# Kernel optimization log

Measured on AMD Instinct MI355X. Metric: run time of the kernel, lower is better.

## Reference

```python
import jax, jax.numpy as jnp
from jax import lax
import numpy as np

AE_THRESHOLD = 0.5


def setup_inputs() -> dict:
    key = jax.random.key(0)
    ks = jax.random.split(key, 8)
    B, C, H, W = 8, 80, 128, 128
    return {
        "tl_heat": jax.random.normal(ks[0], (B, C, H, W), jnp.float32),
        "br_heat": jax.random.normal(ks[1], (B, C, H, W), jnp.float32),
        "ct_heat": jax.random.normal(ks[2], (B, C, H, W), jnp.float32),
        "tl_tag": jax.random.normal(ks[3], (B, 1, H, W), jnp.float32),
        "br_tag": jax.random.normal(ks[4], (B, 1, H, W), jnp.float32),
        "tl_regr": jax.random.normal(ks[5], (B, 2, H, W), jnp.float32),
        "br_regr": jax.random.normal(ks[6], (B, 2, H, W), jnp.float32),
        "ct_regr": jax.random.normal(ks[7], (B, 2, H, W), jnp.float32),
        "K": 100,
        "kernel": 3,
        "num_dets": 1000,
    }


def _nms(heat, kernel):
    # maxpool NMS: keep only local maxima (SAME padding, stride 1, NCHW)
    hmax = lax.reduce_window(heat, -jnp.inf, lax.max,
                             (1, 1, kernel, kernel), (1, 1, 1, 1), 'SAME')
    return heat * (hmax == heat).astype(heat.dtype)


def _topk(scores, K):
    B, C, H, W = scores.shape
    s, inds = lax.top_k(scores.reshape(B, -1), K)  # over cat*H*W
    clses = inds // (H * W)
    inds = inds % (H * W)
    ys = (inds // W).astype(jnp.float32)
    xs = (inds % W).astype(jnp.float32)
    return s, inds, clses, ys, xs


def _gather(feat, inds):
    # NCHW -> (B, H*W, C), gather spatial rows by inds (B, K) -> (B, K, C)
    B, C, H, W = feat.shape
    f = feat.transpose(0, 2, 3, 1).reshape(B, H * W, C)
    return jnp.take_along_axis(f, inds[:, :, None], axis=1)


def reference(tl_heat, br_heat, ct_heat, tl_tag, br_tag,
              tl_regr, br_regr, ct_regr, K, kernel, num_dets):
    B, C, H, W = tl_heat.shape

    tl_heat = _nms(jax.nn.sigmoid(tl_heat), kernel)
    br_heat = _nms(jax.nn.sigmoid(br_heat), kernel)
    ct_heat = _nms(jax.nn.sigmoid(ct_heat), kernel)

    tl_s, tl_inds, tl_clses, tl_ys, tl_xs = _topk(tl_heat, K)
    br_s, br_inds, br_clses, br_ys, br_xs = _topk(br_heat, K)
    ct_s, ct_inds, ct_clses, ct_ys, ct_xs = _topk(ct_heat, K)

    tl_off = _gather(tl_regr, tl_inds)  # (B, K, 2)
    br_off = _gather(br_regr, br_inds)
    ct_off = _gather(ct_regr, ct_inds)

    # corner coords with sub-pixel offsets; broadcast to (B, K, K) pairs
    tl_xs_p = (tl_xs + tl_off[..., 0])[:, :, None]  # (B, K, 1)
    tl_ys_p = (tl_ys + tl_off[..., 1])[:, :, None]
    br_xs_p = (br_xs + br_off[..., 0])[:, None, :]  # (B, 1, K)
    br_ys_p = (br_ys + br_off[..., 1])[:, None, :]
    ct_xs_p = ct_xs + ct_off[..., 0]                # (B, K)
    ct_ys_p = ct_ys + ct_off[..., 1]

    pair = (B, K, K)
    bboxes = jnp.stack([jnp.broadcast_to(tl_xs_p, pair),
                        jnp.broadcast_to(tl_ys_p, pair),
                        jnp.broadcast_to(br_xs_p, pair),
                        jnp.broadcast_to(br_ys_p, pair)], axis=-1)  # (B,K,K,4)

    tl_emb = _gather(tl_tag, tl_inds)[:, :, 0]  # (B, K)
    br_emb = _gather(br_tag, br_inds)[:, :, 0]
    dists = jnp.abs(tl_emb[:, :, None] - br_emb[:, None, :])  # (B,K,K)

    scores = (tl_s[:, :, None] + br_s[:, None, :]) * 0.5
    reject = ((tl_clses[:, :, None] != br_clses[:, None, :])
              | (dists > AE_THRESHOLD)
              | (br_xs_p < tl_xs_p)
              | (br_ys_p < tl_ys_p))
    scores = jnp.where(reject, -jnp.ones_like(scores), scores)

    scores, inds = lax.top_k(scores.reshape(B, -1), num_dets)  # (B, num_dets)

    bboxes = jnp.take_along_axis(bboxes.reshape(B, K * K, 4),
                                 inds[:, :, None], axis=1)
    clses_full = jnp.broadcast_to(tl_clses[:, :, None], pair).reshape(B, K * K)
    clses = jnp.take_along_axis(clses_full, inds, axis=1).astype(jnp.float32)
    tl_s_full = jnp.broadcast_to(tl_s[:, :, None], pair).reshape(B, K * K)
    br_s_full = jnp.broadcast_to(br_s[:, None, :], pair).reshape(B, K * K)
    tl_sc = jnp.take_along_axis(tl_s_full, inds, axis=1)
    br_sc = jnp.take_along_axis(br_s_full, inds, axis=1)

    detections = jnp.concatenate([bboxes, scores[..., None], tl_sc[..., None],
                                  br_sc[..., None], clses[..., None]], axis=-1)
    center = jnp.stack([ct_xs_p, ct_ys_p,
                        ct_clses.astype(jnp.float32), ct_s], axis=-1)  # (B,K,4)
    return detections, center
```

## Files before the change

kernel.cpp:

```cpp
#include <hip/hip_runtime.h>
#include <cstdint>

#define NB    8
#define NC    80
#define HH    128
#define WW    128
#define HW    16384
#define CHW   1310720
#define KTOP  100
#define NDET  1000
#define NPAIR 10000
#define CAP   4096
#define ACAP  2048
#define NBINS 4096
#define VTHR  3.5f

#define OFF_CCNT   0
#define OFF_CCNT2  3072
#define OFF_HIST   6144
#define ZERO_BYTES 399360
#define OFF_THR    399360
#define OFF_CAND   399488
#define OFF_CS     1185920
#define OFF_CX     1195520
#define OFF_CY     1205120
#define OFF_CE     1214720
#define OFF_CCLS   1224320
#define WS_NEEDED  1233920

__device__ __forceinline__ float sigmoidf(float x) {
    float e = expf(-fabsf(x));
    return (x >= 0.f ? 1.f : e) / (1.f + e);
}

__global__ void __launch_bounds__(256) k_nms(
        const float* __restrict__ tl, const float* __restrict__ br,
        const float* __restrict__ ct,
        uint64_t* __restrict__ cand, int* __restrict__ ccnt) {
    __shared__ float lds[34 * WW];

    int tid = threadIdx.x;
    int bid = blockIdx.x;
    int bc = bid / 320;
    int rem_b = bid - bc * 320;
    int chan = rem_b >> 2;
    int q = rem_b & 3;
    int t = bc >> 3; int b = bc & 7;
    const float* heat = (t == 0) ? tl : (t == 1) ? br : ct;
    const float* cb = heat + (size_t)b * CHW + (size_t)chan * HW;
    int ybase = q * 32;
    const float NEG = -__builtin_inff();

    #define GADDR(K, GY) ({ int r_ = (K) >> 5; (GY) = ybase - 1 + r_; \
                            int gyc_ = min(max((GY), 0), HH - 1); \
                            cb + gyc_ * WW + (((K) & 31) << 2); })
    int gy0, gy1, gy2, gy3, gy4 = 0;
    const float* a0 = GADDR(tid,        gy0);
    const float* a1 = GADDR(tid + 256,  gy1);
    const float* a2 = GADDR(tid + 512,  gy2);
    const float* a3 = GADDR(tid + 768,  gy3);
    float4 v0 = *(const float4*)a0;
    float4 v1 = *(const float4*)a1;
    float4 v2 = *(const float4*)a2;
    float4 v3 = *(const float4*)a3;
    float4 v4 = make_float4(0.f, 0.f, 0.f, 0.f);
    if (tid < 64) { const float* a4 = GADDR(tid + 1024, gy4); v4 = *(const float4*)a4; }
    #undef GADDR
    #define PIN(v) asm volatile("" : "+v"(v.x), "+v"(v.y), "+v"(v.z), "+v"(v.w))
    PIN(v0); PIN(v1); PIN(v2); PIN(v3); PIN(v4);
    #undef PIN

    #define STORE(K, V, GY) { \
        float4 vv = (V); \
        if ((GY) < 0 || (GY) > HH - 1) vv = make_float4(NEG, NEG, NEG, NEG); \
        *(float4*)&lds[(((K) >> 5) * WW) + (((K) & 31) << 2)] = vv; }
    STORE(tid,        v0, gy0)
    STORE(tid + 256,  v1, gy1)
    STORE(tid + 512,  v2, gy2)
    STORE(tid + 768,  v3, gy3)
    if (tid < 64) STORE(tid + 1024, v4, gy4)
    #undef STORE
    __syncthreads();

    int rg = tid >> 5;
    int tile_x = (tid & 31) << 2;
    int lrow = 1 + rg * 4;
    float4 A = *(const float4*)&lds[(lrow - 1) * WW + tile_x];
    float4 B = *(const float4*)&lds[lrow * WW + tile_x];
    int ccbase = bc * 32;
    uint64_t* cd = cand + (size_t)bc * CAP;
    int ibase = chan * HW + (ybase + rg * 4) * WW + tile_x;

    #pragma unroll
    for (int j = 0; j < 4; ++j) {
        float4 C = *(const float4*)&lds[(lrow + j + 1) * WW + tile_x];
        float c0 = fmaxf(fmaxf(A.x, B.x), C.x);
        float c1 = fmaxf(fmaxf(A.y, B.y), C.y);
        float c2 = fmaxf(fmaxf(A.z, B.z), C.z);
        float c3 = fmaxf(fmaxf(A.w, B.w), C.w);
        float cl = __shfl_up(c3, 1);
        float cr = __shfl_down(c0, 1);
        if (tile_x == 0)      cl = NEG;
        if (tile_x == WW - 4) cr = NEG;
        float w0 = fmaxf(fmaxf(cl, c0), c1);
        float w1 = fmaxf(fmaxf(c0, c1), c2);
        float w2 = fmaxf(fmaxf(c1, c2), c3);
        float w3 = fmaxf(fmaxf(c2, c3), cr);

        #define EMIT(Wm, V, P) \
            if ((Wm) == (V) && (V) >= VTHR) { \
                uint32_t bt = __float_as_uint(sigmoidf(V)); \
                int pos = atomicAdd(&ccnt[ccbase], 1); \
                if (pos < CAP) \
                    cd[pos] = ((uint64_t)bt << 32) | \
                              (uint32_t)(~(uint32_t)(ibase + j * WW + (P))); \
            }
        EMIT(w0, B.x, 0)
        EMIT(w1, B.y, 1)
        EMIT(w2, B.z, 2)
        EMIT(w3, B.w, 3)
        #undef EMIT
        A = B; B = C;
    }
}

__device__ uint64_t key_at(const float* __restrict__ hb, int i) {
    float v = hb[i];
    int rem = i & (HW - 1);
    int y = rem >> 7, x = rem & (WW - 1);
    bool mx = true;
    if (y > 0) {
        if (x > 0      && hb[i - WW - 1] > v) mx = false;
        if (              hb[i - WW    ] > v) mx = false;
        if (x < WW - 1 && hb[i - WW + 1] > v) mx = false;
    }
    if (x > 0      && hb[i - 1] > v) mx = false;
    if (x < WW - 1 && hb[i + 1] > v) mx = false;
    if (y < HH - 1) {
        if (x > 0      && hb[i + WW - 1] > v) mx = false;
        if (              hb[i + WW    ] > v) mx = false;
        if (x < WW - 1 && hb[i + WW + 1] > v) mx = false;
    }
    if (!mx) return 0;
    return ((uint64_t)__float_as_uint(sigmoidf(v)) << 32) | (uint32_t)(~(uint32_t)i);
}

__device__ __forceinline__ bool fast_ok(const int* ccnt, int bc) {
    int n = ccnt[bc * 32];
    return (n >= KTOP) && (n <= CAP);
}

__global__ void __launch_bounds__(256) fb_hist(
        const int* __restrict__ ccnt,
        const float* __restrict__ tl, const float* __restrict__ br,
        const float* __restrict__ ct, uint32_t* __restrict__ hist) {
    int bc = blockIdx.y;
    if (fast_ok(ccnt, bc)) return;
    __shared__ uint32_t lh[NBINS];
    for (int i = threadIdx.x; i < NBINS; i += 256) lh[i] = 0;
    __syncthreads();
    int t = bc >> 3; int b = bc & 7;
    const float* heat = (t == 0) ? tl : (t == 1) ? br : ct;
    const float* hb = heat + (size_t)b * CHW;
    for (int i = blockIdx.x * 256 + threadIdx.x; i < CHW; i += 32 * 256) {
        uint64_t k = key_at(hb, i);
        if (k) atomicAdd(&lh[(uint32_t)(k >> 51)], 1u);
    }
    __syncthreads();
    uint32_t* gh = hist + (size_t)bc * NBINS;
    for (int i = threadIdx.x; i < NBINS; i += 256) {
        uint32_t c = lh[i];
        if (c) atomicAdd(&gh[i], c);
    }
}

__global__ void __launch_bounds__(256) fb_thresh(
        const int* __restrict__ ccnt, const uint32_t* __restrict__ hist,
        int* __restrict__ thr) {
    int bc = blockIdx.x;
    if (fast_ok(ccnt, bc)) return;
    __shared__ uint32_t csum[256];
    const uint32_t* h = hist + (size_t)bc * NBINS;
    int tid = threadIdx.x;
    uint32_t bins[16];
    #pragma unroll
    for (int i = 0; i < 16; ++i) bins[i] = h[tid * 16 + i];
    if (tid == 0) bins[0] = 0;
    uint32_t s = 0;
    #pragma unroll
    for (int i = 0; i < 16; ++i) s += bins[i];
    csum[tid] = s;
    __syncthreads();
    for (int step = 1; step < 256; step <<= 1) {
        uint32_t add = (tid + step < 256) ? csum[tid + step] : 0;
        __syncthreads();
        csum[tid] += add;
        __syncthreads();
    }
    uint32_t inc = csum[tid];
    uint32_t above = (tid + 1 < 256) ? csum[tid + 1] : 0;
    if (tid == 0 && inc < KTOP) thr[bc] = 1;
    if (above < KTOP && inc >= KTOP) {
        uint32_t cum = above;
        int T = 1;
        #pragma unroll
        for (int i = 15; i >= 0; --i) {
            cum += bins[i];
            if (cum >= KTOP) { T = tid * 16 + i; break; }
        }
        thr[bc] = T;
    }
}

__global__ void __launch_bounds__(256) fb_collect(
        const int* __restrict__ ccnt, const int* __restrict__ thr,
        const float* __restrict__ tl, const float* __restrict__ br,
        const float* __restrict__ ct,
        uint64_t* __restrict__ cand, int* __restrict__ ccnt2) {
    int bc = blockIdx.y;
    if (fast_ok(ccnt, bc)) return;
    int t = bc >> 3; int b = bc & 7;
    const float* heat = (t == 0) ? tl : (t == 1) ? br : ct;
    const float* hb = heat + (size_t)b * CHW;
    int T = thr[bc];
    for (int i = blockIdx.x * 256 + threadIdx.x; i < CHW; i += 32 * 256) {
        uint64_t k = key_at(hb, i);
        if (k && (int)(uint32_t)(k >> 51) >= T) {
            int pc = atomicAdd(&ccnt2[bc * 32], 1);
            if (pc < CAP) cand[(size_t)bc * CAP + pc] = k;
        }
    }
}

template <int N>
__device__ void bitonic_desc(uint64_t* k) {
    for (int kk = 2; kk <= N; kk <<= 1) {
        for (int j = kk >> 1; j > 0; j >>= 1) {
            __syncthreads();
            for (int i = threadIdx.x; i < N; i += blockDim.x) {
                int l = i ^ j;
                if (l > i) {
                    uint64_t a = k[i], b = k[l];
                    bool up = ((i & kk) == 0);
                    if (up ? (a < b) : (a > b)) { k[i] = b; k[l] = a; }
                }
            }
        }
    }
    __syncthreads();
}

__global__ void __launch_bounds__(1024) k_select(
        const uint64_t* __restrict__ cand, const int* __restrict__ ccnt,
        const int* __restrict__ ccnt2,
        const float* __restrict__ tl_tag, const float* __restrict__ br_tag,
        const float* __restrict__ tl_regr, const float* __restrict__ br_regr,
        const float* __restrict__ ct_regr,
        float* __restrict__ cs, float* __restrict__ cx, float* __restrict__ cy,
        float* __restrict__ ce, int* __restrict__ ccls) {
    __shared__ uint64_t keys[CAP];
    int bc = blockIdx.x; int t = bc >> 3; int b = bc & 7;
    int nf = ccnt[bc * 32];
    bool ok = (nf >= KTOP) && (nf <= CAP);
    int n = ok ? nf : ccnt2[bc * 32];
    if (n > CAP) n = CAP;
    if (n <= 512) {
        for (int i = threadIdx.x; i < 512; i += 1024)
            keys[i] = (i < n) ? cand[(size_t)bc * CAP + i] : 0ull;
        bitonic_desc<512>(keys);
    } else if (n <= 2048) {
        for (int i = threadIdx.x; i < 2048; i += 1024)
            keys[i] = (i < n) ? cand[(size_t)bc * CAP + i] : 0ull;
        bitonic_desc<2048>(keys);
    } else {
        for (int i = threadIdx.x; i < CAP; i += 1024)
            keys[i] = (i < n) ? cand[(size_t)bc * CAP + i] : 0ull;
        bitonic_desc<CAP>(keys);
    }
    if (threadIdx.x < KTOP) {
        uint64_t key = keys[threadIdx.x];
        float s = __uint_as_float((uint32_t)(key >> 32));
        uint32_t idx = ~(uint32_t)key;
        int cls = (int)(idx >> 14);
        int rem = (int)(idx & (HW - 1));
        int y = rem >> 7, x = rem & (WW - 1);
        const float* regr = (t == 0) ? tl_regr : (t == 1) ? br_regr : ct_regr;
        float o0 = regr[((size_t)b * 2 + 0) * HW + rem];
        float o1 = regr[((size_t)b * 2 + 1) * HW + rem];
        float emb = 0.f;
        if (t == 0) emb = tl_tag[(size_t)b * HW + rem];
        else if (t == 1) emb = br_tag[(size_t)b * HW + rem];
        int o = bc * KTOP + threadIdx.x;
        cs[o] = s;
        cx[o] = (float)x + o0;
        cy[o] = (float)y + o1;
        ce[o] = emb;
        ccls[o] = cls;
    }
}

__global__ void __launch_bounds__(1024) k_pairfinal(
        const float* __restrict__ cs, const float* __restrict__ cx,
        const float* __restrict__ cy, const float* __restrict__ ce,
        const int* __restrict__ ccls, float* __restrict__ out) {
    int b = blockIdx.x;
    __shared__ float ts[KTOP], tx[KTOP], ty[KTOP], te[KTOP];
    __shared__ int   tc[KTOP];
    __shared__ float bs_[KTOP], bx[KTOP], by[KTOP], be[KTOP];
    __shared__ int   bcl[KTOP];
    __shared__ uint64_t acc[ACAP];
    __shared__ int aidx[ACAP];
    __shared__ int acnt_s;
    int tid = threadIdx.x;
    if (tid == 0) acnt_s = 0;
    if (tid < KTOP) {
        int o = (0 * NB + b) * KTOP + tid;
        ts[tid] = cs[o]; tx[tid] = cx[o]; ty[tid] = cy[o]; te[tid] = ce[o]; tc[tid] = ccls[o];
    } else if (tid >= 512 && tid < 512 + KTOP) {
        int k = tid - 512;
        int o = (1 * NB + b) * KTOP + k;
        bs_[k] = cs[o]; bx[k] = cx[o]; by[k] = cy[o]; be[k] = ce[o]; bcl[k] = ccls[o];
    }
    __syncthreads();
    for (int p = tid; p < NPAIR; p += 1024) {
        int i = p / KTOP, j = p - i * KTOP;
        bool rej = (tc[i] != bcl[j])
                 | (fabsf(te[i] - be[j]) > 0.5f)
                 | (bx[j] < tx[i])
                 | (by[j] < ty[i]);
        if (!rej) {
            float sc = (ts[i] + bs_[j]) * 0.5f;
            int pos = atomicAdd(&acnt_s, 1);
            if (pos < ACAP)
                acc[pos] = ((uint64_t)__float_as_uint(sc) << 32) | (uint32_t)(~(uint32_t)p);
        }
    }
    __syncthreads();
    int m = acnt_s; if (m > ACAP) m = ACAP;
    if (m <= 256) {
        for (int i = tid; i < 256; i += 1024) if (i >= m) acc[i] = 0;
        bitonic_desc<256>(acc);
    } else {
        for (int i = tid; i < ACAP; i += 1024) if (i >= m) acc[i] = 0;
        bitonic_desc<ACAP>(acc);
    }
    for (int i = tid; i < m; i += 1024) aidx[i] = (int)(~(uint32_t)acc[i]);
    __syncthreads();
    for (int d = tid; d < NDET; d += 1024) {
        int p; float sc;
        if (d < m) {
            p = aidx[d];
            sc = __uint_as_float((uint32_t)(acc[d] >> 32));
        } else {
            int r = d - m;
            int idx = r;
            for (;;) {
                int c = 0;
                for (int a = 0; a < m; ++a) c += (aidx[a] <= idx) ? 1 : 0;
                int ni = r + c;
                if (ni == idx) break;
                idx = ni;
            }
            p = idx; sc = -1.f;
        }
        int i = p / KTOP, j = p - i * KTOP;
        int ot = (0 * NB + b) * KTOP + i;
        int ob = (1 * NB + b) * KTOP + j;
        float* dr = out + ((size_t)b * NDET + d) * 8;
        dr[0] = cx[ot]; dr[1] = cy[ot]; dr[2] = cx[ob]; dr[3] = cy[ob];
        dr[4] = sc; dr[5] = cs[ot]; dr[6] = cs[ob]; dr[7] = (float)ccls[ot];
    }
    if (tid < KTOP) {
        int oc = (2 * NB + b) * KTOP + tid;
        float* cr = out + (size_t)NB * NDET * 8 + ((size_t)b * KTOP + tid) * 4;
        cr[0] = cx[oc]; cr[1] = cy[oc]; cr[2] = (float)ccls[oc]; cr[3] = cs[oc];
    }
}

extern "C" void kernel_launch(void* const* d_in, const int* in_sizes, int n_in,
                              void* d_out, int out_size, void* d_ws, size_t ws_size,
                              hipStream_t stream) {
    const float* tl_heat = (const float*)d_in[0];
    const float* br_heat = (const float*)d_in[1];
    const float* ct_heat = (const float*)d_in[2];
    const float* tl_tag  = (const float*)d_in[3];
    const float* br_tag  = (const float*)d_in[4];
    const float* tl_regr = (const float*)d_in[5];
    const float* br_regr = (const float*)d_in[6];
    const float* ct_regr = (const float*)d_in[7];

    if (ws_size < (size_t)WS_NEEDED) return;

    char* ws = (char*)d_ws;
    int*      ccnt  = (int*)(ws + OFF_CCNT);
    int*      ccnt2 = (int*)(ws + OFF_CCNT2);
    uint32_t* hist  = (uint32_t*)(ws + OFF_HIST);
    int*      thr   = (int*)(ws + OFF_THR);
    uint64_t* cand  = (uint64_t*)(ws + OFF_CAND);
    float*    cs    = (float*)(ws + OFF_CS);
    float*    cx    = (float*)(ws + OFF_CX);
    float*    cy    = (float*)(ws + OFF_CY);
    float*    ce    = (float*)(ws + OFF_CE);
    int*      ccls  = (int*)(ws + OFF_CCLS);

    hipMemsetAsync(ws, 0, ZERO_BYTES, stream);

    k_nms<<<24 * NC * 4, 256, 0, stream>>>(tl_heat, br_heat, ct_heat, cand, ccnt);
    fb_hist<<<dim3(32, 24), 256, 0, stream>>>(ccnt, tl_heat, br_heat, ct_heat, hist);
    fb_thresh<<<24, 256, 0, stream>>>(ccnt, hist, thr);
    fb_collect<<<dim3(32, 24), 256, 0, stream>>>(ccnt, thr,
                                                 tl_heat, br_heat, ct_heat,
                                                 cand, ccnt2);
    k_select<<<24, 1024, 0, stream>>>(cand, ccnt, ccnt2, tl_tag, br_tag,
                                      tl_regr, br_regr, ct_regr,
                                      cs, cx, cy, ce, ccls);
    k_pairfinal<<<NB, 1024, 0, stream>>>(cs, cx, cy, ce, ccls, (float*)d_out);
}
```

Measured before the change: 63.41 us.

## Fuse fallback histogram, threshold and collect into one per-slice block kernel

Replaces the three fallback kernels (global histogram, threshold scan, collect) with one 1024-thread block per batch-heatmap slice. The block builds the histogram in shared memory, scans it to find the threshold, and collects candidates without global histogram atomics. This removes two launches and shrinks the memset, since the histogram and threshold buffers are gone. The cost is far less parallelism when the fallback actually runs (24 blocks instead of 768), but in the common fast path every block exits early.

```diff
diff --git a/kernel.cpp b/kernel.cpp
--- a/kernel.cpp
+++ b/kernel.cpp
@@ -17,16 +17,14 @@
 
 #define OFF_CCNT   0
 #define OFF_CCNT2  3072
-#define OFF_HIST   6144
-#define ZERO_BYTES 399360
-#define OFF_THR    399360
-#define OFF_CAND   399488
-#define OFF_CS     1185920
-#define OFF_CX     1195520
-#define OFF_CY     1205120
-#define OFF_CE     1214720
-#define OFF_CCLS   1224320
-#define WS_NEEDED  1233920
+#define ZERO_BYTES 6144
+#define OFF_CAND   6144
+#define OFF_CS     792576
+#define OFF_CX     802176
+#define OFF_CY     811776
+#define OFF_CE     821376
+#define OFF_CCLS   830976
+#define WS_NEEDED  840576
 
 __device__ __forceinline__ float sigmoidf(float x) {
     float e = expf(-fabsf(x));
@@ -150,80 +148,59 @@
     return (n >= KTOP) && (n <= CAP);
 }
 
-__global__ void __launch_bounds__(256) fb_hist(
+__global__ void __launch_bounds__(1024) fb_all(
         const int* __restrict__ ccnt,
         const float* __restrict__ tl, const float* __restrict__ br,
-        const float* __restrict__ ct, uint32_t* __restrict__ hist) {
-    int bc = blockIdx.y;
+        const float* __restrict__ ct,
+        uint64_t* __restrict__ cand, int* __restrict__ ccnt2) {
+    int bc = blockIdx.x;
     if (fast_ok(ccnt, bc)) return;
     __shared__ uint32_t lh[NBINS];
-    for (int i = threadIdx.x; i < NBINS; i += 256) lh[i] = 0;
-    __syncthreads();
+    __shared__ uint32_t csum[1024];
+    __shared__ int thr_s;
+    int tid = threadIdx.x;
     int t = bc >> 3; int b = bc & 7;
     const float* heat = (t == 0) ? tl : (t == 1) ? br : ct;
     const float* hb = heat + (size_t)b * CHW;
-    for (int i = blockIdx.x * 256 + threadIdx.x; i < CHW; i += 32 * 256) {
+
+    for (int i = tid; i < NBINS; i += 1024) lh[i] = 0;
+    __syncthreads();
+    for (int i = tid; i < CHW; i += 1024) {
         uint64_t k = key_at(hb, i);
         if (k) atomicAdd(&lh[(uint32_t)(k >> 51)], 1u);
     }
     __syncthreads();
-    uint32_t* gh = hist + (size_t)bc * NBINS;
-    for (int i = threadIdx.x; i < NBINS; i += 256) {
-        uint32_t c = lh[i];
-        if (c) atomicAdd(&gh[i], c);
-    }
-}
-
-__global__ void __launch_bounds__(256) fb_thresh(
-        const int* __restrict__ ccnt, const uint32_t* __restrict__ hist,
-        int* __restrict__ thr) {
-    int bc = blockIdx.x;
-    if (fast_ok(ccnt, bc)) return;
-    __shared__ uint32_t csum[256];
-    const uint32_t* h = hist + (size_t)bc * NBINS;
-    int tid = threadIdx.x;
-    uint32_t bins[16];
+
+    uint32_t bins[4];
     #pragma unroll
-    for (int i = 0; i < 16; ++i) bins[i] = h[tid * 16 + i];
+    for (int i = 0; i < 4; ++i) bins[i] = lh[tid * 4 + i];
     if (tid == 0) bins[0] = 0;
-    uint32_t s = 0;
-    #pragma unroll
-    for (int i = 0; i < 16; ++i) s += bins[i];
+    uint32_t s = bins[0] + bins[1] + bins[2] + bins[3];
     csum[tid] = s;
     __syncthreads();
-    for (int step = 1; step < 256; step <<= 1) {
-        uint32_t add = (tid + step < 256) ? csum[tid + step] : 0;
+    for (int step = 1; step < 1024; step <<= 1) {
+        uint32_t add = (tid + step < 1024) ? csum[tid + step] : 0;
         __syncthreads();
         csum[tid] += add;
         __syncthreads();
     }
     uint32_t inc = csum[tid];
-    uint32_t above = (tid + 1 < 256) ? csum[tid + 1] : 0;
-    if (tid == 0 && inc < KTOP) thr[bc] = 1;
-    if (above < KTOP && inc >= KTOP) {
+    uint32_t above = (tid < 1023) ? csum[tid + 1] : 0;
+    if (tid == 0 && (int)inc < KTOP) thr_s = 1;
+    if ((int)above < KTOP && (int)inc >= KTOP) {
         uint32_t cum = above;
         int T = 1;
         #pragma unroll
-        for (int i = 15; i >= 0; --i) {
+        for (int i = 3; i >= 0; --i) {
             cum += bins[i];
-            if (cum >= KTOP) { T = tid * 16 + i; break; }
-        }
-        thr[bc] = T;
-    }
-}
-
-__global__ void __launch_bounds__(256) fb_collect(
-        const int* __restrict__ ccnt, const int* __restrict__ thr,
-        const float* __restrict__ tl, const float* __restrict__ br,
-        const float* __restrict__ ct,
-        uint64_t* __restrict__ cand, int* __restrict__ ccnt2) {
-    int bc = blockIdx.y;
-    if (fast_ok(ccnt, bc)) return;
-    int t = bc >> 3; int b = bc & 7;
-    const float* heat = (t == 0) ? tl : (t == 1) ? br : ct;
-    const float* hb = heat + (size_t)b * CHW;
-    int T = thr[bc];
-    for (int i = blockIdx.x * 256 + threadIdx.x; i < CHW; i += 32 * 256) {
+            if ((int)cum >= KTOP) { T = tid * 4 + i; break; }
+        }
+        thr_s = T;
+    }
+    __syncthreads();
+    int T = thr_s;
+
+    for (int i = tid; i < CHW; i += 1024) {
         uint64_t k = key_at(hb, i);
         if (k && (int)(uint32_t)(k >> 51) >= T) {
             int pc = atomicAdd(&ccnt2[bc * 32], 1);
@@ -394,8 +371,6 @@
     char* ws = (char*)d_ws;
     int*      ccnt  = (int*)(ws + OFF_CCNT);
     int*      ccnt2 = (int*)(ws + OFF_CCNT2);
-    uint32_t* hist  = (uint32_t*)(ws + OFF_HIST);
-    int*      thr   = (int*)(ws + OFF_THR);
     uint64_t* cand  = (uint64_t*)(ws + OFF_CAND);
     float*    cs    = (float*)(ws + OFF_CS);
     float*    cx    = (float*)(ws + OFF_CX);
@@ -406,11 +381,7 @@
     hipMemsetAsync(ws, 0, ZERO_BYTES, stream);
 
     k_nms<<<24 * NC * 4, 256, 0, stream>>>(tl_heat, br_heat, ct_heat, cand, ccnt);
-    fb_hist<<<dim3(32, 24), 256, 0, stream>>>(ccnt, tl_heat, br_heat, ct_heat, hist);
-    fb_thresh<<<24, 256, 0, stream>>>(ccnt, hist, thr);
-    fb_collect<<<dim3(32, 24), 256, 0, stream>>>(ccnt, thr,
-                                                 tl_heat, br_heat, ct_heat,
-                                                 cand, ccnt2);
+    fb_all<<<24, 1024, 0, stream>>>(ccnt, tl_heat, br_heat, ct_heat, cand, ccnt2);
     k_select<<<24, 1024, 0, stream>>>(cand, ccnt, ccnt2, tl_tag, br_tag,
                                       tl_regr, br_regr, ct_regr,
                                       cs, cx, cy, ce, ccls);
```

New measurement: 59.49 us. 6.2% less time.
